# Performance work log

Measured on AMD Instinct MI355X. Metric: run time of the kernel, lower is better.

## Reference

```python
import jax, jax.numpy as jnp
import numpy as np

EPS = 1e-5

def setup_inputs() -> dict:
    key = jax.random.key(0)
    k1, k2 = jax.random.split(key)
    x = jax.random.normal(k1, (32, 256, 56, 56), dtype=jnp.float32)
    # Conv2d(in=2, out=1, k=7, bias=False) weight: [out, in, kh, kw]
    conv_w = jax.random.normal(k2, (1, 2, 7, 7), dtype=jnp.float32) * 0.1
    # BatchNorm2d(1) params/buffers (eval mode)
    gamma = jnp.ones((1,), dtype=jnp.float32)
    beta = jnp.zeros((1,), dtype=jnp.float32)
    running_mean = jnp.zeros((1,), dtype=jnp.float32)
    running_var = jnp.ones((1,), dtype=jnp.float32)
    return {"x": x, "conv_w": conv_w, "gamma": gamma, "beta": beta,
            "running_mean": running_mean, "running_var": running_var}

def reference(x, conv_w, gamma, beta, running_mean, running_var):
    # channel-wise max & mean -> [B,2,H,W]
    max_result = jnp.max(x, axis=1, keepdims=True)
    avg_result = jnp.mean(x, axis=1, keepdims=True)
    result = jnp.concatenate([max_result, avg_result], axis=1)
    # 7x7 conv, pad=3, NCHW / OIHW
    out = jax.lax.conv_general_dilated(
        result, conv_w, window_strides=(1, 1), padding=((3, 3), (3, 3)),
        dimension_numbers=("NCHW", "OIHW", "NCHW"))
    # BatchNorm2d(1), eval mode with running stats
    inv = gamma / jnp.sqrt(running_var + EPS)
    out = (out - running_mean[None, :, None, None]) * inv[None, :, None, None] + beta[None, :, None, None]
    gate = jax.nn.sigmoid(out)  # [B,1,H,W]
    return x * gate
```

## Files before the change

kernel.cpp:

```cpp
#include <hip/hip_runtime.h>
#include <math.h>

#define NB 32
#define NC 256
#define SH 56
#define SW 56
#define HW 3136
#define HW4 784
#define PERB4 (NC * HW4)
#define NCG 8

__device__ __forceinline__ float4 max4(float4 a, float4 b) {
    return make_float4(fmaxf(a.x,b.x), fmaxf(a.y,b.y), fmaxf(a.z,b.z), fmaxf(a.w,b.w));
}
__device__ __forceinline__ float4 add4(float4 a, float4 b) {
    return make_float4(a.x+b.x, a.y+b.y, a.z+b.z, a.w+b.w);
}

__global__ __launch_bounds__(256) void k_reduce_lin(const float4* __restrict__ x,
                                                    float4* __restrict__ pmax,
                                                    float4* __restrict__ psum) {
    const int tid  = threadIdx.x;
    const int bid  = blockIdx.x;
    const int half = bid & 1;
    const int bcg  = bid >> 1;
    const float4* base = x + (size_t)bcg * (32 * HW4) + half * 392;

    const float NEG = -__builtin_inff();
    float4 m0 = make_float4(NEG,NEG,NEG,NEG), s0 = make_float4(0,0,0,0);
    float4 m1 = m0, s1 = s0;
    #pragma unroll 4
    for (int c = 0; c < 32; ++c) {
        const float4 v0 = base[c * HW4 + tid];
        m0 = max4(m0, v0); s0 = add4(s0, v0);
        if (tid < 136) {
            const float4 v1 = base[c * HW4 + 256 + tid];
            m1 = max4(m1, v1); s1 = add4(s1, v1);
        }
    }
    const size_t obase = (size_t)bcg * HW4 + half * 392;
    pmax[obase + tid] = m0;
    psum[obase + tid] = s0;
    if (tid < 136) {
        pmax[obase + 256 + tid] = m1;
        psum[obase + 256 + tid] = s1;
    }
}

__global__ __launch_bounds__(256) void k_gate_mul(const float4* __restrict__ pmax,
                                                  const float4* __restrict__ psum,
                                                  const float* __restrict__ cw,
                                                  const float* __restrict__ gamma,
                                                  const float* __restrict__ beta,
                                                  const float* __restrict__ rmean,
                                                  const float* __restrict__ rvar,
                                                  const float4* __restrict__ x,
                                                  float4* __restrict__ out) {
    __shared__ float sw[99];
    __shared__ __align__(16) float smx[8 * SW];
    __shared__ __align__(16) float sav[8 * SW];
    __shared__ float4 sgate4[28];

    const int tid = threadIdx.x;
    const int b  = blockIdx.x / 28;
    const int rp = blockIdx.x - b * 28;

    const float inv = gamma[0] * rsqrtf(rvar[0] + 1e-5f);
    if (tid < 98) sw[tid] = cw[tid] * inv;
    if (tid == 0) sw[98] = beta[0] - rmean[0] * inv;

    const int r0  = 2 * rp - 3;
    const int rlo = r0 > 0 ? r0 : 0;
    const int rhi = (2 * rp + 4) < (SH - 1) ? (2 * rp + 4) : (SH - 1);
    const int n4  = (rhi - rlo + 1) * 14;
    const int sh4 = (rlo - r0) * 14;

    if (tid < n4) {
        const size_t pb = (size_t)(b * NCG) * HW4 + rlo * 14 + tid;
        float4 m = pmax[pb];
        #pragma unroll
        for (int cg = 1; cg < NCG; ++cg) m = max4(m, pmax[pb + (size_t)cg * HW4]);
        ((float4*)smx)[sh4 + tid] = m;
    } else if (tid >= 128 && tid - 128 < n4) {
        const int t = tid - 128;
        const size_t pb = (size_t)(b * NCG) * HW4 + rlo * 14 + t;
        float4 s = psum[pb];
        #pragma unroll
        for (int cg = 1; cg < NCG; ++cg) s = add4(s, psum[pb + (size_t)cg * HW4]);
        const float r = 1.0f / 256.0f;
        s.x *= r; s.y *= r; s.z *= r; s.w *= r;
        ((float4*)sav)[sh4 + t] = s;
    }
    __syncthreads();

    if (tid < 112) {
        const int lr = tid >= 56 ? 1 : 0;
        const int w  = tid - lr * 56;
        const int hr = 2 * rp + lr;
        float acc = sw[98];
        #pragma unroll
        for (int kh = 0; kh < 7; ++kh) {
            const int hh = hr + kh - 3;
            if (hh < 0 || hh >= SH) continue;
            const int slot = lr + kh;
            #pragma unroll
            for (int kw = 0; kw < 7; ++kw) {
                const int ww = w + kw - 3;
                if (ww < 0 || ww >= SW) continue;
                acc += smx[slot * SW + ww] * sw[kh * 7 + kw]
                     + sav[slot * SW + ww] * sw[49 + kh * 7 + kw];
            }
        }
        ((float*)sgate4)[tid] = 1.0f / (1.0f + expf(-acc));
    }
    __syncthreads();

    const size_t strip = (size_t)b * PERB4 + (size_t)rp * 28;
    #pragma unroll 4
    for (int it = 0; it < 28; ++it) {
        const unsigned idx = (unsigned)it * 256u + (unsigned)tid;
        const unsigned c = idx / 28u;
        const unsigned q = idx - c * 28u;
        const size_t off = strip + (size_t)c * HW4 + q;
        const float4 g  = sgate4[q];
        const float4 xv = x[off];
        out[off] = make_float4(xv.x * g.x, xv.y * g.y, xv.z * g.z, xv.w * g.w);
    }
}

extern "C" void kernel_launch(void* const* d_in, const int* in_sizes, int n_in,
                              void* d_out, int out_size, void* d_ws, size_t ws_size,
                              hipStream_t stream) {
    const float* x     = (const float*)d_in[0];
    const float* cw    = (const float*)d_in[1];
    const float* gamma = (const float*)d_in[2];
    const float* beta  = (const float*)d_in[3];
    const float* rmean = (const float*)d_in[4];
    const float* rvar  = (const float*)d_in[5];
    float* out = (float*)d_out;

    float4* pmax = (float4*)d_ws;
    float4* psum = pmax + (size_t)NB * NCG * HW4;

    k_reduce_lin<<<NB * NCG * 2, 256, 0, stream>>>((const float4*)x, pmax, psum);

    k_gate_mul<<<NB * 28, 256, 0, stream>>>(
        pmax, psum, cw, gamma, beta, rmean, rvar,
        (const float4*)x, (float4*)out);
}
```

Baseline: 63.85 us.

## Fuse channel reduction, conv gate, and multiply into single strip kernel

Replaces the two-kernel pipeline (partial channel reduction into workspace, then gate and multiply) with one kernel per batch and 7-row strip. Each block recomputes the max and mean over all channels for its rows plus the 3-row halo, runs the 7x7 conv and sigmoid, then scales its strip. This removes the workspace round trip and one launch. In exchange it re-reads halo rows across strips and uses far fewer blocks with a long serial channel loop.

```diff
diff --git a/kernel.cpp b/kernel.cpp
--- a/kernel.cpp
+++ b/kernel.cpp
@@ -8,7 +8,8 @@
 #define HW 3136
 #define HW4 784
 #define PERB4 (NC * HW4)
-#define NCG 8
+#define SROWS 7
+#define STRIPS 8
 
 __device__ __forceinline__ float4 max4(float4 a, float4 b) {
     return make_float4(fmaxf(a.x,b.x), fmaxf(a.y,b.y), fmaxf(a.z,b.z), fmaxf(a.w,b.w));
@@ -17,112 +18,83 @@
     return make_float4(a.x+b.x, a.y+b.y, a.z+b.z, a.w+b.w);
 }
 
-__global__ __launch_bounds__(256) void k_reduce_lin(const float4* __restrict__ x,
-                                                    float4* __restrict__ pmax,
-                                                    float4* __restrict__ psum) {
-    const int tid  = threadIdx.x;
-    const int bid  = blockIdx.x;
-    const int half = bid & 1;
-    const int bcg  = bid >> 1;
-    const float4* base = x + (size_t)bcg * (32 * HW4) + half * 392;
-
-    const float NEG = -__builtin_inff();
-    float4 m0 = make_float4(NEG,NEG,NEG,NEG), s0 = make_float4(0,0,0,0);
-    float4 m1 = m0, s1 = s0;
-    #pragma unroll 4
-    for (int c = 0; c < 32; ++c) {
-        const float4 v0 = base[c * HW4 + tid];
-        m0 = max4(m0, v0); s0 = add4(s0, v0);
-        if (tid < 136) {
-            const float4 v1 = base[c * HW4 + 256 + tid];
-            m1 = max4(m1, v1); s1 = add4(s1, v1);
-        }
-    }
-    const size_t obase = (size_t)bcg * HW4 + half * 392;
-    pmax[obase + tid] = m0;
-    psum[obase + tid] = s0;
-    if (tid < 136) {
-        pmax[obase + 256 + tid] = m1;
-        psum[obase + 256 + tid] = s1;
-    }
-}
-
-__global__ __launch_bounds__(256) void k_gate_mul(const float4* __restrict__ pmax,
-                                                  const float4* __restrict__ psum,
-                                                  const float* __restrict__ cw,
-                                                  const float* __restrict__ gamma,
-                                                  const float* __restrict__ beta,
-                                                  const float* __restrict__ rmean,
-                                                  const float* __restrict__ rvar,
-                                                  const float4* __restrict__ x,
-                                                  float4* __restrict__ out) {
+__global__ __launch_bounds__(256) void k_strip(const float4* __restrict__ x,
+                                               const float* __restrict__ cw,
+                                               const float* __restrict__ gamma,
+                                               const float* __restrict__ beta,
+                                               const float* __restrict__ rmean,
+                                               const float* __restrict__ rvar,
+                                               float4* __restrict__ out) {
     __shared__ float sw[99];
-    __shared__ __align__(16) float smx[8 * SW];
-    __shared__ __align__(16) float sav[8 * SW];
-    __shared__ float4 sgate4[28];
+    __shared__ __align__(16) float smx[13 * SW];
+    __shared__ __align__(16) float sav[13 * SW];
+    __shared__ __align__(16) float sgate[SROWS * SW];
 
     const int tid = threadIdx.x;
-    const int b  = blockIdx.x / 28;
-    const int rp = blockIdx.x - b * 28;
+    const int b   = blockIdx.x >> 3;
+    const int s   = blockIdx.x & 7;
+    const int r0  = s * SROWS;
+    const int h0  = (r0 - 3) > 0 ? (r0 - 3) : 0;
+    const int h1  = (r0 + 9) < (SH - 1) ? (r0 + 9) : (SH - 1);
+    const int nf4 = (h1 - h0 + 1) * 14;
 
     const float inv = gamma[0] * rsqrtf(rvar[0] + 1e-5f);
     if (tid < 98) sw[tid] = cw[tid] * inv;
     if (tid == 0) sw[98] = beta[0] - rmean[0] * inv;
 
-    const int r0  = 2 * rp - 3;
-    const int rlo = r0 > 0 ? r0 : 0;
-    const int rhi = (2 * rp + 4) < (SH - 1) ? (2 * rp + 4) : (SH - 1);
-    const int n4  = (rhi - rlo + 1) * 14;
-    const int sh4 = (rlo - r0) * 14;
-
-    if (tid < n4) {
-        const size_t pb = (size_t)(b * NCG) * HW4 + rlo * 14 + tid;
-        float4 m = pmax[pb];
-        #pragma unroll
-        for (int cg = 1; cg < NCG; ++cg) m = max4(m, pmax[pb + (size_t)cg * HW4]);
-        ((float4*)smx)[sh4 + tid] = m;
-    } else if (tid >= 128 && tid - 128 < n4) {
-        const int t = tid - 128;
-        const size_t pb = (size_t)(b * NCG) * HW4 + rlo * 14 + t;
-        float4 s = psum[pb];
-        #pragma unroll
-        for (int cg = 1; cg < NCG; ++cg) s = add4(s, psum[pb + (size_t)cg * HW4]);
+    if (tid < nf4) {
+        const float4* base = x + (size_t)b * PERB4 + h0 * 14 + tid;
+        const float NEG = -__builtin_inff();
+        float4 m = make_float4(NEG, NEG, NEG, NEG);
+        float4 sm = make_float4(0.f, 0.f, 0.f, 0.f);
+        #pragma unroll 8
+        for (int c = 0; c < NC; ++c) {
+            const float4 v = base[(size_t)c * HW4];
+            m = max4(m, v);
+            sm = add4(sm, v);
+        }
         const float r = 1.0f / 256.0f;
-        s.x *= r; s.y *= r; s.z *= r; s.w *= r;
-        ((float4*)sav)[sh4 + t] = s;
+        sm.x *= r; sm.y *= r; sm.z *= r; sm.w *= r;
+        ((float4*)smx)[tid] = m;
+        ((float4*)sav)[tid] = sm;
     }
     __syncthreads();
 
-    if (tid < 112) {
-        const int lr = tid >= 56 ? 1 : 0;
-        const int w  = tid - lr * 56;
-        const int hr = 2 * rp + lr;
-        float acc = sw[98];
+    if (tid < 196) {
         #pragma unroll
-        for (int kh = 0; kh < 7; ++kh) {
-            const int hh = hr + kh - 3;
-            if (hh < 0 || hh >= SH) continue;
-            const int slot = lr + kh;
+        for (int e = 0; e < 2; ++e) {
+            const int px = 2 * tid + e;
+            const int lr = px / SW;
+            const int w  = px - lr * SW;
+            const int h  = r0 + lr;
+            float acc = sw[98];
             #pragma unroll
-            for (int kw = 0; kw < 7; ++kw) {
-                const int ww = w + kw - 3;
-                if (ww < 0 || ww >= SW) continue;
-                acc += smx[slot * SW + ww] * sw[kh * 7 + kw]
-                     + sav[slot * SW + ww] * sw[49 + kh * 7 + kw];
+            for (int kh = 0; kh < 7; ++kh) {
+                const int hh = h + kh - 3;
+                if (hh < 0 || hh >= SH) continue;
+                const int slot = hh - h0;
+                #pragma unroll
+                for (int kw = 0; kw < 7; ++kw) {
+                    const int ww = w + kw - 3;
+                    if (ww < 0 || ww >= SW) continue;
+                    acc += smx[slot * SW + ww] * sw[kh * 7 + kw]
+                         + sav[slot * SW + ww] * sw[49 + kh * 7 + kw];
+                }
             }
+            sgate[px] = 1.0f / (1.0f + expf(-acc));
         }
-        ((float*)sgate4)[tid] = 1.0f / (1.0f + expf(-acc));
     }
     __syncthreads();
 
-    const size_t strip = (size_t)b * PERB4 + (size_t)rp * 28;
+    const float4* sg4 = (const float4*)sgate;
+    const size_t sbase = (size_t)b * PERB4 + r0 * 14;
     #pragma unroll 4
-    for (int it = 0; it < 28; ++it) {
+    for (int it = 0; it < 98; ++it) {
         const unsigned idx = (unsigned)it * 256u + (unsigned)tid;
-        const unsigned c = idx / 28u;
-        const unsigned q = idx - c * 28u;
-        const size_t off = strip + (size_t)c * HW4 + q;
-        const float4 g  = sgate4[q];
+        const unsigned c = idx / 98u;
+        const unsigned q = idx - c * 98u;
+        const size_t off = sbase + (size_t)c * HW4 + q;
+        const float4 g  = sg4[q];
         const float4 xv = x[off];
         out[off] = make_float4(xv.x * g.x, xv.y * g.y, xv.z * g.z, xv.w * g.w);
     }
@@ -131,20 +103,14 @@
 extern "C" void kernel_launch(void* const* d_in, const int* in_sizes, int n_in,
                               void* d_out, int out_size, void* d_ws, size_t ws_size,
                               hipStream_t stream) {
-    const float* x     = (const float*)d_in[0];
+    const float4* x4   = (const float4*)d_in[0];
     const float* cw    = (const float*)d_in[1];
     const float* gamma = (const float*)d_in[2];
     const float* beta  = (const float*)d_in[3];
     const float* rmean = (const float*)d_in[4];
     const float* rvar  = (const float*)d_in[5];
-    float* out = (float*)d_out;
+    float4* out4 = (float4*)d_out;
 
-    float4* pmax = (float4*)d_ws;
-    float4* psum = pmax + (size_t)NB * NCG * HW4;
-
-    k_reduce_lin<<<NB * NCG * 2, 256, 0, stream>>>((const float4*)x, pmax, psum);
-
-    k_gate_mul<<<NB * 28, 256, 0, stream>>>(
-        pmax, psum, cw, gamma, beta, rmean, rvar,
-        (const float4*)x, (float4*)out);
+    k_strip<<<NB * STRIPS, 256, 0, stream>>>(
+        x4, cw, gamma, beta, rmean, rvar, out4);
 }
```

Result: slower. 68.58 us (+7.4%).
